# Performance work log

Hardware: AMD Instinct MI355X
Metric: run time of the kernel (lower is better)

## Reference

```python
import jax, jax.numpy as jnp
import numpy as np

N = 100_000   # nodes
E = 1_600_000 # edges
G = 128       # graphs in batch
DIN, DOUT = 100, 200


def setup_inputs() -> dict:
    key = jax.random.key(0)
    ks = jax.random.split(key, 12)
    def lin_w(k, fan_in, fan_out):
        return (jax.random.normal(k, (fan_in, fan_out), jnp.float32) / np.sqrt(fan_in)).astype(jnp.float32)
    return {
        "x": jax.random.normal(ks[0], (N, DIN), jnp.float32),
        "edge_index": jax.random.randint(ks[1], (2, E), 0, N, dtype=jnp.int32),
        "batch": jnp.sort(jax.random.randint(ks[2], (N,), 0, G, dtype=jnp.int32)),
        "W1": lin_w(ks[3], DIN, DOUT),  "b1": jnp.zeros((DOUT,), jnp.float32),
        "Wc": lin_w(ks[4], DOUT, DOUT), "bc": jnp.zeros((DOUT,), jnp.float32),
        "W2": lin_w(ks[5], DOUT, DOUT), "b2": jnp.zeros((DOUT,), jnp.float32),
        "W3": lin_w(ks[6], DOUT, DOUT), "b3": jnp.zeros((DOUT,), jnp.float32),
        "Wcls": lin_w(ks[7], DOUT, 2),  "bcls": jnp.zeros((2,), jnp.float32),
    }


def gcn_conv(x, W, b, src, dst, n_nodes):
    """PyG GCNConv: D^{-1/2}(A+I)D^{-1/2} X W + b, symmetric norm with self-loops."""
    h = x @ W  # [N, Dout]
    # degree at targets including the self-loop (+1)
    deg = jax.ops.segment_sum(jnp.ones((src.shape[0],), x.dtype), dst, num_segments=n_nodes) + 1.0
    dinv = jax.lax.rsqrt(deg)  # [N]
    # gather -> normalize -> scatter-add (messages along edges)
    msg = h[src] * (dinv[src] * dinv[dst])[:, None]          # [E, Dout]
    agg = jax.ops.segment_sum(msg, dst, num_segments=n_nodes)  # [N, Dout]
    # self-loop contribution handled analytically: norm_ii = dinv[i]^2
    agg = agg + h * (dinv * dinv)[:, None]
    return agg + b


def reference(x, edge_index, batch, W1, b1, Wc, bc, W2, b2, W3, b3, Wcls, bcls):
    src, dst = edge_index[0], edge_index[1]
    h = jax.nn.relu(gcn_conv(x, W1, b1, src, dst, N))
    # dropout is identity at eval time
    h = h @ Wc + bc
    h = jax.nn.relu(gcn_conv(h, W2, b2, src, dst, N))
    h = gcn_conv(h, W3, b3, src, dst, N)
    pooled = jax.ops.segment_max(h, batch, num_segments=G)  # global max pool -> [G, Dout]
    logits = pooled @ Wcls + bcls
    return jax.nn.softmax(logits, axis=1)
```

## Files before the change

### kernel.cpp

```cpp
#include <hip/hip_runtime.h>
#include <stdint.h>

#define N_NODES 100000
#define N_EDGES 1600000
#define N_GRAPHS 128
#define DIN 100
#define DOUT 200
#define LDH 200
#define LDX 128

#define NB 391
#define BCAP 5120
#define EPB 2048
#define NBLK 782

typedef unsigned short u16;
typedef unsigned int u32;
typedef _Float16 f16;
typedef f16 half8 __attribute__((ext_vector_type(8)));
typedef f16 half4 __attribute__((ext_vector_type(4)));
typedef f16 half2v __attribute__((ext_vector_type(2)));
typedef float floatx4 __attribute__((ext_vector_type(4)));

__device__ __forceinline__ float h2f(u16 h) {
  f16 x; __builtin_memcpy(&x, &h, 2); return (float)x;
}
__device__ __forceinline__ u16 f2h(float f) {
  f16 x = (f16)f; u16 r; __builtin_memcpy(&r, &x, 2); return r;
}

__device__ __forceinline__ void pack_frag(const float* __restrict__ W, int K, int nfrag,
                                          u16* __restrict__ out, int idx) {
  if (idx >= nfrag) return;
  int lane = idx & 63;
  int t = idx >> 6;
  int ct = t % 13, ks = t / 13;
  int n = ct * 16 + (lane & 15);
  int kbase = ks * 32 + (lane >> 4) * 8;
  u16 v[8];
  #pragma unroll
  for (int j = 0; j < 8; ++j) {
    int k = kbase + j;
    float f = (k < K && n < DOUT) ? W[(size_t)k * DOUT + n] : 0.f;
    v[j] = f2h(f);
  }
  uint4 o;
  o.x = (u32)v[0] | ((u32)v[1] << 16);
  o.y = (u32)v[2] | ((u32)v[3] << 16);
  o.z = (u32)v[4] | ((u32)v[5] << 16);
  o.w = (u32)v[6] | ((u32)v[7] << 16);
  *(uint4*)(out + (size_t)idx * 8) = o;
}

#define B_GB    391
#define B_COMB  549
#define B_PK1   562
#define B_PK3   585
#define B_TOT   (585 + NBLK)
__global__ void k_prep(const int* __restrict__ batch, int* __restrict__ gstart,
                       int* __restrict__ gend, const int* __restrict__ dst,
                       int* __restrict__ histAll,
                       const float* __restrict__ Wc, const float* __restrict__ bc,
                       const float* __restrict__ W2, float* __restrict__ Wc2,
                       float* __restrict__ bc2, const float* __restrict__ W1,
                       const float* __restrict__ W3, u16* __restrict__ Wpk1,
                       u16* __restrict__ Wpk3) {
  int b = blockIdx.x, t = threadIdx.x;
  if (b < B_GB) {
    int i = b * 256 + t;
    if (i >= N_NODES) return;
    int g = batch[i];
    if (i == 0 || batch[i - 1] != g) gstart[g] = i;
    if (i == N_NODES - 1 || batch[i + 1] != g) gend[g] = i;
  } else if (b < B_COMB) {
    int gid = (b - B_GB) * 256 + t;
    if (gid >= 201 * DOUT) return;
    int r = gid / DOUT, c = gid % DOUT;
    const float* a = (r < DOUT) ? (Wc + (size_t)r * DOUT) : bc;
    float s = 0.f;
    for (int k = 0; k < DOUT; ++k) s += a[k] * W2[(size_t)k * DOUT + c];
    if (r < DOUT) Wc2[(size_t)r * DOUT + c] = s;
    else bc2[c] = s;
  } else if (b < B_PK1) {
    pack_frag(W1, DIN, 4 * 13 * 64, Wpk1, (b - B_COMB) * 256 + t);
  } else if (b < B_PK3) {
    pack_frag(W3, DOUT, 7 * 13 * 64, Wpk3, (b - B_PK1) * 256 + t);
  } else {
    __shared__ int hist[NB];
    int hb = b - B_PK3;
    int e0 = hb * EPB;
    int e1 = min(e0 + EPB, N_EDGES);
    for (int j = t; j < NB; j += 256) hist[j] = 0;
    __syncthreads();
    for (int i = e0 + t; i < e1; i += 256)
      atomicAdd(&hist[dst[i] >> 8], 1);
    __syncthreads();
    for (int j = t; j < NB; j += 256)
      histAll[(size_t)hb * NB + j] = hist[j];
  }
}

__global__ void k_scan(const int* __restrict__ histAll, int* __restrict__ baseAll,
                       int* __restrict__ gcur) {
  __shared__ int s[256];
  int j = blockIdx.x, t = threadIdx.x;
  int run = 0;
  for (int c = 0; c < NBLK; c += 256) {
    int idx = c + t;
    int v = (idx < NBLK) ? histAll[(size_t)idx * NB + j] : 0;
    s[t] = v;
    __syncthreads();
    for (int o = 1; o < 256; o <<= 1) {
      int x = (t >= o) ? s[t - o] : 0;
      __syncthreads();
      s[t] += x;
      __syncthreads();
    }
    if (idx < NBLK) baseAll[(size_t)idx * NB + j] = run + s[t] - v;
    run += s[255];
    __syncthreads();
  }
  if (t == 0) gcur[j] = run;
}

__global__ void k_scatter(const int* __restrict__ src, const int* __restrict__ dst,
                          const int* __restrict__ baseAll, uint2* __restrict__ ebuf) {
  __shared__ int cur[NB];
  int b = blockIdx.x, t = threadIdx.x;
  int e0 = b * EPB;
  int e1 = min(e0 + EPB, N_EDGES);
  for (int j = t; j < NB; j += 256) cur[j] = baseAll[(size_t)b * NB + j];
  __syncthreads();
  for (int i = e0 + t; i < e1; i += 256) {
    int d = dst[i];
    int bk = d >> 8;
    int pos = atomicAdd(&cur[bk], 1);
    if (pos < BCAP)
      ebuf[(size_t)bk * BCAP + pos] = make_uint2((u32)d, (u32)src[i]);
  }
}

__global__ void k_csr(const uint2* __restrict__ ebuf, const int* __restrict__ gcur,
                      int* __restrict__ rowptr, float* __restrict__ dinv,
                      int* __restrict__ colv) {
  __shared__ int s_cnt[256];
  __shared__ int s_cur[256];
  __shared__ int s_scan[256];
  __shared__ int s_g[NB];
  __shared__ int s_base;
  int b = blockIdx.x, t = threadIdx.x;
  for (int j = t; j < NB; j += 256) s_g[j] = gcur[j];
  s_cnt[t] = 0;
  __syncthreads();
  if (t == 0) {
    int run = 0;
    for (int i = 0; i < b; ++i) run += s_g[i];
    s_base = run;
    if (b == NB - 1) rowptr[N_NODES] = run + s_g[b];
  }
  __syncthreads();
  int cnt = s_g[b];
  int base = s_base;
  int node0 = b << 8;
  const uint2* eb = ebuf + (size_t)b * BCAP;
  for (int i = t; i < cnt; i += 256)
    atomicAdd(&s_cnt[eb[i].x & 255], 1);
  __syncthreads();
  int v = s_cnt[t];
  s_scan[t] = v;
  __syncthreads();
  for (int o = 1; o < 256; o <<= 1) {
    int x = (t >= o) ? s_scan[t - o] : 0;
    __syncthreads();
    s_scan[t] += x;
    __syncthreads();
  }
  int run = s_scan[t] - v;
  s_cur[t] = base + run;
  int node = node0 + t;
  if (node < N_NODES) {
    rowptr[node] = base + run;
    dinv[node] = rsqrtf((float)v + 1.0f);
  }
  __syncthreads();
  for (int i = t; i < cnt; i += 256) {
    uint2 e = eb[i];
    int pos = atomicAdd(&s_cur[e.x & 255], 1);
    colv[pos] = (int)e.y;
  }
}

#define P_XS  25000
#define P_TOT 25023
__global__ void k_post(const float* __restrict__ x, const float* __restrict__ dinv,
                       u16* __restrict__ xs, const float* __restrict__ Wc2,
                       u16* __restrict__ Wpk2) {
  int b = blockIdx.x, t = threadIdx.x;
  if (b < P_XS) {
    int gid = b * 256 + t;
    int node = gid >> 6, lane = gid & 63;
    if (node >= N_NODES) return;
    if (lane >= 50) {
      int c = 100 + (lane - 50) * 2;
      *(half2v*)(xs + (size_t)node * LDX + c) = half2v{0, 0};
      return;
    }
    float d = dinv[node];
    float2 vv = *(const float2*)(x + (size_t)node * DIN + lane * 2);
    half2v o; o[0] = (f16)(d * vv.x); o[1] = (f16)(d * vv.y);
    *(half2v*)(xs + (size_t)node * LDX + lane * 2) = o;
  } else {
    pack_frag(Wc2, DOUT, 7 * 13 * 64, Wpk2, (b - P_XS) * 256 + t);
  }
}

template <int NKS>
__global__ __launch_bounds__(256) void k_gemm_mfma(const u16* __restrict__ A, int lda,
                                                   const u16* __restrict__ Wpk,
                                                   const float* __restrict__ bias,
                                                   const float* __restrict__ rowscale,
                                                   u16* __restrict__ C, int relu, int nrows) {
  int wv = threadIdx.x >> 6;
  int lane = threadIdx.x & 63;
  int r0 = blockIdx.x * 128 + wv * 32;
  int m = lane & 15, q = lane >> 4;
  int row0 = r0 + m, row1 = r0 + 16 + m;
  bool ok0 = (row0 < nrows), ok1 = (row1 < nrows);
  const u16* a0p = A + (size_t)row0 * lda + q * 8;
  const u16* a1p = A + (size_t)row1 * lda + q * 8;

  floatx4 acc0[13], acc1[13];
  #pragma unroll
  for (int ct = 0; ct < 13; ++ct) {
    acc0[ct] = floatx4{0.f, 0.f, 0.f, 0.f};
    acc1[ct] = floatx4{0.f, 0.f, 0.f, 0.f};
  }

  const u16* wp = Wpk + (size_t)lane * 8;
  #pragma unroll
  for (int ks = 0; ks < NKS; ++ks) {
    half8 a0 = ok0 ? *(const half8*)(a0p + ks * 32) : half8{0, 0, 0, 0, 0, 0, 0, 0};
    half8 a1 = ok1 ? *(const half8*)(a1p + ks * 32) : half8{0, 0, 0, 0, 0, 0, 0, 0};
    #pragma unroll
    for (int ct = 0; ct < 13; ++ct) {
      half8 bfr = *(const half8*)(wp + (size_t)(ks * 13 + ct) * 512);
      acc0[ct] = __builtin_amdgcn_mfma_f32_16x16x32_f16(a0, bfr, acc0[ct], 0, 0, 0);
      acc1[ct] = __builtin_amdgcn_mfma_f32_16x16x32_f16(a1, bfr, acc1[ct], 0, 0, 0);
    }
  }

  float sc0[4], sc1[4];
  #pragma unroll
  for (int rg = 0; rg < 4; ++rg) {
    int or0 = r0 + q * 4 + rg;
    int or1 = r0 + 16 + q * 4 + rg;
    sc0[rg] = (rowscale && or0 < nrows) ? rowscale[or0] : 1.f;
    sc1[rg] = (rowscale && or1 < nrows) ? rowscale[or1] : 1.f;
  }

  #pragma unroll
  for (int ct = 0; ct < 13; ++ct) {
    int c = ct * 16 + m;
    if (c >= DOUT) continue;
    float bv = bias ? bias[c] : 0.f;
    #pragma unroll
    for (int rg = 0; rg < 4; ++rg) {
      int or0 = r0 + q * 4 + rg;
      if (or0 < nrows) {
        float v = acc0[ct][rg] + bv;
        if (relu) v = fmaxf(v, 0.f);
        C[(size_t)or0 * LDH + c] = f2h(v * sc0[rg]);
      }
      int or1 = r0 + 16 + q * 4 + rg;
      if (or1 < nrows) {
        float v = acc1[ct][rg] + bv;
        if (relu) v = fmaxf(v, 0.f);
        C[(size_t)or1 * LDH + c] = f2h(v * sc1[rg]);
      }
    }
  }
}

__global__ void k_agg200h(const u16* __restrict__ T, const float* __restrict__ dinv,
                          const int* __restrict__ rowptr, const int* __restrict__ col,
                          const float* __restrict__ bias, u16* __restrict__ OUT,
                          int relu) {
  int wave = (blockIdx.x * blockDim.x + threadIdx.x) >> 6;
  int lane = threadIdx.x & 63;
  if (wave >= N_NODES || lane >= 50) return;
  int node = wave;
  int c4 = lane * 4;
  int beg = __builtin_amdgcn_readfirstlane(rowptr[node]);
  int end = __builtin_amdgcn_readfirstlane(rowptr[node + 1]);
  half4 sv = *(const half4*)(T + (size_t)node * LDH + c4);
  float di = dinv[node];
  float ax = 0.f, ay = 0.f, az = 0.f, aw = 0.f;
  int e = beg;
  for (; e + 16 <= end; e += 16) {
    int s[16];
    half4 tv[16];
    #pragma unroll
    for (int j = 0; j < 16; ++j) s[j] = col[e + j];
    #pragma unroll
    for (int j = 0; j < 16; ++j)
      tv[j] = *(const half4*)(T + (size_t)s[j] * LDH + c4);
    #pragma unroll
    for (int j = 0; j < 16; ++j) {
      ax += (float)tv[j][0]; ay += (float)tv[j][1];
      az += (float)tv[j][2]; aw += (float)tv[j][3];
    }
  }
  if (e + 8 <= end) {
    int s[8];
    half4 tv[8];
    #pragma unroll
    for (int j = 0; j < 8; ++j) s[j] = col[e + j];
    #pragma unroll
    for (int j = 0; j < 8; ++j)
      tv[j] = *(const half4*)(T + (size_t)s[j] * LDH + c4);
    #pragma unroll
    for (int j = 0; j < 8; ++j) {
      ax += (float)tv[j][0]; ay += (float)tv[j][1];
      az += (float)tv[j][2]; aw += (float)tv[j][3];
    }
    e += 8;
  }
  if (e + 4 <= end) {
    int s[4];
    half4 tv[4];
    #pragma unroll
    for (int j = 0; j < 4; ++j) s[j] = col[e + j];
    #pragma unroll
    for (int j = 0; j < 4; ++j)
      tv[j] = *(const half4*)(T + (size_t)s[j] * LDH + c4);
    #pragma unroll
    for (int j = 0; j < 4; ++j) {
      ax += (float)tv[j][0]; ay += (float)tv[j][1];
      az += (float)tv[j][2]; aw += (float)tv[j][3];
    }
    e += 4;
  }
  for (; e < end; ++e) {
    half4 tv = *(const half4*)(T + (size_t)col[e] * LDH + c4);
    ax += (float)tv[0]; ay += (float)tv[1];
    az += (float)tv[2]; aw += (float)tv[3];
  }
  float rx = di * (ax + (float)sv[0]);
  float ry = di * (ay + (float)sv[1]);
  float rz = di * (az + (float)sv[2]);
  float rw = di * (aw + (float)sv[3]);
  if (bias) {
    rx += bias[c4 + 0]; ry += bias[c4 + 1];
    rz += bias[c4 + 2]; rw += bias[c4 + 3];
  }
  if (relu) {
    rx = fmaxf(rx, 0.f); ry = fmaxf(ry, 0.f);
    rz = fmaxf(rz, 0.f); rw = fmaxf(rw, 0.f);
  }
  half4 o;
  o[0] = (f16)rx; o[1] = (f16)ry; o[2] = (f16)rz; o[3] = (f16)rw;
  __builtin_nontemporal_store(o, (half4*)(OUT + (size_t)node * LDH + c4));
}

__global__ void k_agg100h(const u16* __restrict__ T, const float* __restrict__ dinv,
                          const int* __restrict__ rowptr, const int* __restrict__ col,
                          u16* __restrict__ OUT) {
  int wave = (blockIdx.x * blockDim.x + threadIdx.x) >> 6;
  int lane = threadIdx.x & 63;
  if (wave >= N_NODES) return;
  int node = wave;
  int c2 = lane * 2;
  int beg = __builtin_amdgcn_readfirstlane(rowptr[node]);
  int end = __builtin_amdgcn_readfirstlane(rowptr[node + 1]);
  half2v sv = *(const half2v*)(T + (size_t)node * LDX + c2);
  float di = dinv[node];
  float ax = 0.f, ay = 0.f;
  int e = beg;
  for (; e + 16 <= end; e += 16) {
    int s[16];
    half2v tv[16];
    #pragma unroll
    for (int j = 0; j < 16; ++j) s[j] = col[e + j];
    #pragma unroll
    for (int j = 0; j < 16; ++j)
      tv[j] = *(const half2v*)(T + (size_t)s[j] * LDX + c2);
    #pragma unroll
    for (int j = 0; j < 16; ++j) { ax += (float)tv[j][0]; ay += (float)tv[j][1]; }
  }
  if (e + 8 <= end) {
    int s[8];
    half2v tv[8];
    #pragma unroll
    for (int j = 0; j < 8; ++j) s[j] = col[e + j];
    #pragma unroll
    for (int j = 0; j < 8; ++j)
      tv[j] = *(const half2v*)(T + (size_t)s[j] * LDX + c2);
    #pragma unroll
    for (int j = 0; j < 8; ++j) { ax += (float)tv[j][0]; ay += (float)tv[j][1]; }
    e += 8;
  }
  if (e + 4 <= end) {
    int s[4];
    half2v tv[4];
    #pragma unroll
    for (int j = 0; j < 4; ++j) s[j] = col[e + j];
    #pragma unroll
    for (int j = 0; j < 4; ++j)
      tv[j] = *(const half2v*)(T + (size_t)s[j] * LDX + c2);
    #pragma unroll
    for (int j = 0; j < 4; ++j) { ax += (float)tv[j][0]; ay += (float)tv[j][1]; }
    e += 4;
  }
  for (; e < end; ++e) {
    half2v tv = *(const half2v*)(T + (size_t)col[e] * LDX + c2);
    ax += (float)tv[0]; ay += (float)tv[1];
  }
  half2v o;
  o[0] = (f16)(di * (ax + (float)sv[0]));
  o[1] = (f16)(di * (ay + (float)sv[1]));
  __builtin_nontemporal_store(o, (half2v*)(OUT + (size_t)node * LDX + c2));
}

#define POOL_CHUNKS 8
__global__ void k_pool1h(const u16* __restrict__ H, const int* __restrict__ gstart,
                         const int* __restrict__ gend, float* __restrict__ part) {
  int g = blockIdx.x, c = blockIdx.y, t = threadIdx.x;
  if (t >= DOUT) return;
  int s = gstart[g], e = gend[g];
  float m = -3.4e38f;
  if (s >= 0 && e >= s && e < N_NODES) {
    int len = e - s + 1;
    int cs = s + (int)(((long long)len * c) / POOL_CHUNKS);
    int ce = s + (int)(((long long)len * (c + 1)) / POOL_CHUNKS);
    for (int i = cs; i < ce; ++i) m = fmaxf(m, h2f(H[(size_t)i * LDH + t]));
  }
  part[(size_t)(g * POOL_CHUNKS + c) * DOUT + t] = m;
}

__global__ void k_poolcls(const float* __restrict__ part, const float* __restrict__ Wcls,
                          const float* __restrict__ bcls, float* __restrict__ out) {
  __shared__ float l0s[256], l1s[256];
  int g = blockIdx.x, t = threadIdx.x;
  float c0 = 0.f, c1 = 0.f;
  if (t < DOUT) {
    float m = -3.4e38f;
    #pragma unroll
    for (int c = 0; c < POOL_CHUNKS; ++c)
      m = fmaxf(m, part[(size_t)(g * POOL_CHUNKS + c) * DOUT + t]);
    c0 = m * Wcls[t * 2 + 0];
    c1 = m * Wcls[t * 2 + 1];
  }
  l0s[t] = c0; l1s[t] = c1;
  __syncthreads();
  for (int o = 128; o > 0; o >>= 1) {
    if (t < o) { l0s[t] += l0s[t + o]; l1s[t] += l1s[t + o]; }
    __syncthreads();
  }
  if (t == 0) {
    float l0 = l0s[0] + bcls[0], l1 = l1s[0] + bcls[1];
    float m = fmaxf(l0, l1);
    float e0 = expf(l0 - m), e1 = expf(l1 - m);
    float inv = 1.0f / (e0 + e1);
    out[g * 2 + 0] = e0 * inv;
    out[g * 2 + 1] = e1 * inv;
  }
}

static inline size_t align256(size_t x) { return (x + 255) & ~(size_t)255; }

extern "C" void kernel_launch(void* const* d_in, const int* in_sizes, int n_in,
                              void* d_out, int out_size, void* d_ws, size_t ws_size,
                              hipStream_t stream) {
  const float* x     = (const float*)d_in[0];
  const int*   ei    = (const int*)d_in[1];
  const int*   batch = (const int*)d_in[2];
  const float* W1    = (const float*)d_in[3];
  const float* b1    = (const float*)d_in[4];
  const float* Wc    = (const float*)d_in[5];
  const float* bc    = (const float*)d_in[6];
  const float* W2    = (const float*)d_in[7];
  const float* b2    = (const float*)d_in[8];
  const float* W3    = (const float*)d_in[9];
  const float* b3    = (const float*)d_in[10];
  const float* Wcls  = (const float*)d_in[11];
  const float* bcls  = (const float*)d_in[12];
  float* out = (float*)d_out;

  const int N = N_NODES, E = N_EDGES;
  const int* src = ei;
  const int* dst = ei + E;

  char* ws = (char*)d_ws;
  size_t off = 0;
  float* dinv    = (float*)(ws + off); off = align256(off + (size_t)N * 4);
  int*   rowptr  = (int*)  (ws + off); off = align256(off + (size_t)(N + 1) * 4);
  int*   col     = (int*)  (ws + off); off = align256(off + (size_t)E * 4);
  int*   gcur    = (int*)  (ws + off); off = align256(off + (size_t)NB * 4);
  int*   histAll = (int*)  (ws + off); off = align256(off + (size_t)NBLK * NB * 4);
  int*   baseAll = (int*)  (ws + off); off = align256(off + (size_t)NBLK * NB * 4);
  int*   gstart  = (int*)  (ws + off); off = align256(off + 512);
  int*   gend    = (int*)  (ws + off); off = align256(off + 512);
  float* Wc2     = (float*)(ws + off); off = align256(off + (size_t)DOUT * DOUT * 4);
  float* bc2     = (float*)(ws + off); off = align256(off + (size_t)DOUT * 4);
  u16*   Wpk1    = (u16*)  (ws + off); off = align256(off + (size_t)4 * 13 * 64 * 8 * 2);
  u16*   Wpk2    = (u16*)  (ws + off); off = align256(off + (size_t)7 * 13 * 64 * 8 * 2);
  u16*   Wpk3    = (u16*)  (ws + off); off = align256(off + (size_t)7 * 13 * 64 * 8 * 2);
  u16*   xs      = (u16*)  (ws + off); off = align256(off + ((size_t)N * LDX + 128) * 2);
  u16*   bufX    = (u16*)  (ws + off); off = align256(off + ((size_t)N * LDX + 128) * 2);
  u16*   buf0    = (u16*)  (ws + off); off = align256(off + ((size_t)N * LDH + 128) * 2);
  u16*   buf1    = (u16*)  (ws + off); off = align256(off + ((size_t)N * LDH + 128) * 2);
  u16*   buf2    = (u16*)  (ws + off); off = align256(off + ((size_t)N * LDH + 128) * 2);

  uint2* ebuf = (uint2*)buf0;
  float* part = (float*)buf1;

  k_prep<<<B_TOT, 256, 0, stream>>>(batch, gstart, gend, dst, histAll,
                                    Wc, bc, W2, Wc2, bc2, W1, W3, Wpk1, Wpk3);
  k_scan<<<NB, 256, 0, stream>>>(histAll, baseAll, gcur);
  k_scatter<<<NBLK, 256, 0, stream>>>(src, dst, baseAll, ebuf);
  k_csr<<<NB, 256, 0, stream>>>(ebuf, gcur, rowptr, dinv, col);
  k_post<<<P_TOT, 256, 0, stream>>>(x, dinv, xs, Wc2, Wpk2);

  int gemmb = (N + 127) / 128;
  int aggb  = (N + 3) / 4;

  k_agg100h<<<aggb, 256, 0, stream>>>(xs, dinv, rowptr, col, bufX);
  k_gemm_mfma<4><<<gemmb, 256, 0, stream>>>(bufX, LDX, Wpk1, b1, nullptr, buf0, 1, N);
  k_gemm_mfma<7><<<gemmb, 256, 0, stream>>>(buf0, LDH, Wpk2, bc2, dinv, buf2, 0, N);
  k_agg200h<<<aggb, 256, 0, stream>>>(buf2, dinv, rowptr, col, b2, buf0, 1);
  k_gemm_mfma<7><<<gemmb, 256, 0, stream>>>(buf0, LDH, Wpk3, nullptr, dinv, buf1, 0, N);
  k_agg200h<<<aggb, 256, 0, stream>>>(buf1, dinv, rowptr, col, b3, buf2, 0);

  dim3 pg(N_GRAPHS, POOL_CHUNKS);
  k_pool1h<<<pg, 256, 0, stream>>>(buf2, gstart, gend, part);
  k_poolcls<<<N_GRAPHS, 256, 0, stream>>>(part, Wcls, bcls, out);
}
```

Before: 662.6 us.

## Process four nodes per wave in aggregation and parallelize CSR base sum

Each aggregation wave now handles four consecutive nodes. It loads their row pointers with one per-lane read and broadcasts them with readlane, which cuts wave count and per-node launch and setup overhead. The serial prefix sum for the CSR block base becomes a block-wide tree reduction. Pooling reads half2 pairs per thread. The zero-fill of padding columns in the scaled input is dropped, and aggregation lanes 50 and up now exit early, so padding columns in xs and bufX are never written. Those columns may then hold garbage that reaches the first GEMM, and NaN garbage multiplied by zero weights would still give NaN.

```diff
diff --git a/kernel.cpp b/kernel.cpp
--- a/kernel.cpp
+++ b/kernel.cpp
@@ -147,20 +147,22 @@
   __shared__ int s_cur[256];
   __shared__ int s_scan[256];
   __shared__ int s_g[NB];
-  __shared__ int s_base;
+  __shared__ int s_red[256];
   int b = blockIdx.x, t = threadIdx.x;
   for (int j = t; j < NB; j += 256) s_g[j] = gcur[j];
   s_cnt[t] = 0;
   __syncthreads();
-  if (t == 0) {
-    int run = 0;
-    for (int i = 0; i < b; ++i) run += s_g[i];
-    s_base = run;
-    if (b == NB - 1) rowptr[N_NODES] = run + s_g[b];
-  }
-  __syncthreads();
+  int pacc = 0;
+  for (int i = t; i < b; i += 256) pacc += s_g[i];
+  s_red[t] = pacc;
+  __syncthreads();
+  for (int o = 128; o > 0; o >>= 1) {
+    if (t < o) s_red[t] += s_red[t + o];
+    __syncthreads();
+  }
+  int base = s_red[0];
+  if (b == NB - 1 && t == 0) rowptr[N_NODES] = base + s_g[b];
   int cnt = s_g[b];
-  int base = s_base;
   int node0 = b << 8;
   const uint2* eb = ebuf + (size_t)b * BCAP;
   for (int i = t; i < cnt; i += 256)
@@ -199,12 +201,7 @@
   if (b < P_XS) {
     int gid = b * 256 + t;
     int node = gid >> 6, lane = gid & 63;
-    if (node >= N_NODES) return;
-    if (lane >= 50) {
-      int c = 100 + (lane - 50) * 2;
-      *(half2v*)(xs + (size_t)node * LDX + c) = half2v{0, 0};
-      return;
-    }
+    if (node >= N_NODES || lane >= 50) return;
     float d = dinv[node];
     float2 vv = *(const float2*)(x + (size_t)node * DIN + lane * 2);
     half2v o; o[0] = (f16)(d * vv.x); o[1] = (f16)(d * vv.y);
@@ -287,79 +284,84 @@
                           int relu) {
   int wave = (blockIdx.x * blockDim.x + threadIdx.x) >> 6;
   int lane = threadIdx.x & 63;
-  if (wave >= N_NODES || lane >= 50) return;
-  int node = wave;
+  int n0 = wave * 4;
+  if (n0 >= N_NODES) return;
+  int rpl = rowptr[n0 + (lane < 4 ? lane : 4)];
+  if (lane >= 50) return;
   int c4 = lane * 4;
-  int beg = __builtin_amdgcn_readfirstlane(rowptr[node]);
-  int end = __builtin_amdgcn_readfirstlane(rowptr[node + 1]);
-  half4 sv = *(const half4*)(T + (size_t)node * LDH + c4);
-  float di = dinv[node];
-  float ax = 0.f, ay = 0.f, az = 0.f, aw = 0.f;
-  int e = beg;
-  for (; e + 16 <= end; e += 16) {
-    int s[16];
-    half4 tv[16];
-    #pragma unroll
-    for (int j = 0; j < 16; ++j) s[j] = col[e + j];
-    #pragma unroll
-    for (int j = 0; j < 16; ++j)
-      tv[j] = *(const half4*)(T + (size_t)s[j] * LDH + c4);
-    #pragma unroll
-    for (int j = 0; j < 16; ++j) {
-      ax += (float)tv[j][0]; ay += (float)tv[j][1];
-      az += (float)tv[j][2]; aw += (float)tv[j][3];
-    }
-  }
-  if (e + 8 <= end) {
-    int s[8];
-    half4 tv[8];
-    #pragma unroll
-    for (int j = 0; j < 8; ++j) s[j] = col[e + j];
-    #pragma unroll
-    for (int j = 0; j < 8; ++j)
-      tv[j] = *(const half4*)(T + (size_t)s[j] * LDH + c4);
-    #pragma unroll
-    for (int j = 0; j < 8; ++j) {
-      ax += (float)tv[j][0]; ay += (float)tv[j][1];
-      az += (float)tv[j][2]; aw += (float)tv[j][3];
-    }
-    e += 8;
-  }
-  if (e + 4 <= end) {
-    int s[4];
-    half4 tv[4];
-    #pragma unroll
-    for (int j = 0; j < 4; ++j) s[j] = col[e + j];
-    #pragma unroll
-    for (int j = 0; j < 4; ++j)
-      tv[j] = *(const half4*)(T + (size_t)s[j] * LDH + c4);
-    #pragma unroll
-    for (int j = 0; j < 4; ++j) {
-      ax += (float)tv[j][0]; ay += (float)tv[j][1];
-      az += (float)tv[j][2]; aw += (float)tv[j][3];
-    }
-    e += 4;
-  }
-  for (; e < end; ++e) {
-    half4 tv = *(const half4*)(T + (size_t)col[e] * LDH + c4);
-    ax += (float)tv[0]; ay += (float)tv[1];
-    az += (float)tv[2]; aw += (float)tv[3];
-  }
-  float rx = di * (ax + (float)sv[0]);
-  float ry = di * (ay + (float)sv[1]);
-  float rz = di * (az + (float)sv[2]);
-  float rw = di * (aw + (float)sv[3]);
-  if (bias) {
-    rx += bias[c4 + 0]; ry += bias[c4 + 1];
-    rz += bias[c4 + 2]; rw += bias[c4 + 3];
-  }
-  if (relu) {
-    rx = fmaxf(rx, 0.f); ry = fmaxf(ry, 0.f);
-    rz = fmaxf(rz, 0.f); rw = fmaxf(rw, 0.f);
-  }
-  half4 o;
-  o[0] = (f16)rx; o[1] = (f16)ry; o[2] = (f16)rz; o[3] = (f16)rw;
-  __builtin_nontemporal_store(o, (half4*)(OUT + (size_t)node * LDH + c4));
+  for (int i = 0; i < 4; ++i) {
+    int node = n0 + i;
+    int beg = __builtin_amdgcn_readlane(rpl, i);
+    int end = __builtin_amdgcn_readlane(rpl, i + 1);
+    half4 sv = *(const half4*)(T + (size_t)node * LDH + c4);
+    float di = dinv[node];
+    float ax = 0.f, ay = 0.f, az = 0.f, aw = 0.f;
+    int e = beg;
+    for (; e + 16 <= end; e += 16) {
+      int s[16];
+      half4 tv[16];
+      #pragma unroll
+      for (int j = 0; j < 16; ++j) s[j] = col[e + j];
+      #pragma unroll
+      for (int j = 0; j < 16; ++j)
+        tv[j] = *(const half4*)(T + (size_t)s[j] * LDH + c4);
+      #pragma unroll
+      for (int j = 0; j < 16; ++j) {
+        ax += (float)tv[j][0]; ay += (float)tv[j][1];
+        az += (float)tv[j][2]; aw += (float)tv[j][3];
+      }
+    }
+    if (e + 8 <= end) {
+      int s[8];
+      half4 tv[8];
+      #pragma unroll
+      for (int j = 0; j < 8; ++j) s[j] = col[e + j];
+      #pragma unroll
+      for (int j = 0; j < 8; ++j)
+        tv[j] = *(const half4*)(T + (size_t)s[j] * LDH + c4);
+      #pragma unroll
+      for (int j = 0; j < 8; ++j) {
+        ax += (float)tv[j][0]; ay += (float)tv[j][1];
+        az += (float)tv[j][2]; aw += (float)tv[j][3];
+      }
+      e += 8;
+    }
+    if (e + 4 <= end) {
+      int s[4];
+      half4 tv[4];
+      #pragma unroll
+      for (int j = 0; j < 4; ++j) s[j] = col[e + j];
+      #pragma unroll
+      for (int j = 0; j < 4; ++j)
+        tv[j] = *(const half4*)(T + (size_t)s[j] * LDH + c4);
+      #pragma unroll
+      for (int j = 0; j < 4; ++j) {
+        ax += (float)tv[j][0]; ay += (float)tv[j][1];
+        az += (float)tv[j][2]; aw += (float)tv[j][3];
+      }
+      e += 4;
+    }
+    for (; e < end; ++e) {
+      half4 tv = *(const half4*)(T + (size_t)col[e] * LDH + c4);
+      ax += (float)tv[0]; ay += (float)tv[1];
+      az += (float)tv[2]; aw += (float)tv[3];
+    }
+    float rx = di * (ax + (float)sv[0]);
+    float ry = di * (ay + (float)sv[1]);
+    float rz = di * (az + (float)sv[2]);
+    float rw = di * (aw + (float)sv[3]);
+    if (bias) {
+      rx += bias[c4 + 0]; ry += bias[c4 + 1];
+      rz += bias[c4 + 2]; rw += bias[c4 + 3];
+    }
+    if (relu) {
+      rx = fmaxf(rx, 0.f); ry = fmaxf(ry, 0.f);
+      rz = fmaxf(rz, 0.f); rw = fmaxf(rw, 0.f);
+    }
+    half4 o;
+    o[0] = (f16)rx; o[1] = (f16)ry; o[2] = (f16)rz; o[3] = (f16)rw;
+    __builtin_nontemporal_store(o, (half4*)(OUT + (size_t)node * LDH + c4));
+  }
 }
 
 __global__ void k_agg100h(const u16* __restrict__ T, const float* __restrict__ dinv,
@@ -367,74 +369,85 @@
                           u16* __restrict__ OUT) {
   int wave = (blockIdx.x * blockDim.x + threadIdx.x) >> 6;
   int lane = threadIdx.x & 63;
-  if (wave >= N_NODES) return;
-  int node = wave;
+  int n0 = wave * 4;
+  if (n0 >= N_NODES) return;
+  int rpl = rowptr[n0 + (lane < 4 ? lane : 4)];
+  if (lane >= 50) return;
   int c2 = lane * 2;
-  int beg = __builtin_amdgcn_readfirstlane(rowptr[node]);
-  int end = __builtin_amdgcn_readfirstlane(rowptr[node + 1]);
-  half2v sv = *(const half2v*)(T + (size_t)node * LDX + c2);
-  float di = dinv[node];
-  float ax = 0.f, ay = 0.f;
-  int e = beg;
-  for (; e + 16 <= end; e += 16) {
-    int s[16];
-    half2v tv[16];
-    #pragma unroll
-    for (int j = 0; j < 16; ++j) s[j] = col[e + j];
-    #pragma unroll
-    for (int j = 0; j < 16; ++j)
-      tv[j] = *(const half2v*)(T + (size_t)s[j] * LDX + c2);
-    #pragma unroll
-    for (int j = 0; j < 16; ++j) { ax += (float)tv[j][0]; ay += (float)tv[j][1]; }
-  }
-  if (e + 8 <= end) {
-    int s[8];
-    half2v tv[8];
-    #pragma unroll
-    for (int j = 0; j < 8; ++j) s[j] = col[e + j];
-    #pragma unroll
-    for (int j = 0; j < 8; ++j)
-      tv[j] = *(const half2v*)(T + (size_t)s[j] * LDX + c2);
-    #pragma unroll
-    for (int j = 0; j < 8; ++j) { ax += (float)tv[j][0]; ay += (float)tv[j][1]; }
-    e += 8;
-  }
-  if (e + 4 <= end) {
-    int s[4];
-    half2v tv[4];
-    #pragma unroll
-    for (int j = 0; j < 4; ++j) s[j] = col[e + j];
-    #pragma unroll
-    for (int j = 0; j < 4; ++j)
-      tv[j] = *(const half2v*)(T + (size_t)s[j] * LDX + c2);
-    #pragma unroll
-    for (int j = 0; j < 4; ++j) { ax += (float)tv[j][0]; ay += (float)tv[j][1]; }
-    e += 4;
-  }
-  for (; e < end; ++e) {
-    half2v tv = *(const half2v*)(T + (size_t)col[e] * LDX + c2);
-    ax += (float)tv[0]; ay += (float)tv[1];
-  }
-  half2v o;
-  o[0] = (f16)(di * (ax + (float)sv[0]));
-  o[1] = (f16)(di * (ay + (float)sv[1]));
-  __builtin_nontemporal_store(o, (half2v*)(OUT + (size_t)node * LDX + c2));
+  for (int i = 0; i < 4; ++i) {
+    int node = n0 + i;
+    int beg = __builtin_amdgcn_readlane(rpl, i);
+    int end = __builtin_amdgcn_readlane(rpl, i + 1);
+    half2v sv = *(const half2v*)(T + (size_t)node * LDX + c2);
+    float di = dinv[node];
+    float ax = 0.f, ay = 0.f;
+    int e = beg;
+    for (; e + 16 <= end; e += 16) {
+      int s[16];
+      half2v tv[16];
+      #pragma unroll
+      for (int j = 0; j < 16; ++j) s[j] = col[e + j];
+      #pragma unroll
+      for (int j = 0; j < 16; ++j)
+        tv[j] = *(const half2v*)(T + (size_t)s[j] * LDX + c2);
+      #pragma unroll
+      for (int j = 0; j < 16; ++j) { ax += (float)tv[j][0]; ay += (float)tv[j][1]; }
+    }
+    if (e + 8 <= end) {
+      int s[8];
+      half2v tv[8];
+      #pragma unroll
+      for (int j = 0; j < 8; ++j) s[j] = col[e + j];
+      #pragma unroll
+      for (int j = 0; j < 8; ++j)
+        tv[j] = *(const half2v*)(T + (size_t)s[j] * LDX + c2);
+      #pragma unroll
+      for (int j = 0; j < 8; ++j) { ax += (float)tv[j][0]; ay += (float)tv[j][1]; }
+      e += 8;
+    }
+    if (e + 4 <= end) {
+      int s[4];
+      half2v tv[4];
+      #pragma unroll
+      for (int j = 0; j < 4; ++j) s[j] = col[e + j];
+      #pragma unroll
+      for (int j = 0; j < 4; ++j)
+        tv[j] = *(const half2v*)(T + (size_t)s[j] * LDX + c2);
+      #pragma unroll
+      for (int j = 0; j < 4; ++j) { ax += (float)tv[j][0]; ay += (float)tv[j][1]; }
+      e += 4;
+    }
+    for (; e < end; ++e) {
+      half2v tv = *(const half2v*)(T + (size_t)col[e] * LDX + c2);
+      ax += (float)tv[0]; ay += (float)tv[1];
+    }
+    half2v o;
+    o[0] = (f16)(di * (ax + (float)sv[0]));
+    o[1] = (f16)(di * (ay + (float)sv[1]));
+    __builtin_nontemporal_store(o, (half2v*)(OUT + (size_t)node * LDX + c2));
+  }
 }
 
 #define POOL_CHUNKS 8
 __global__ void k_pool1h(const u16* __restrict__ H, const int* __restrict__ gstart,
                          const int* __restrict__ gend, float* __restrict__ part) {
   int g = blockIdx.x, c = blockIdx.y, t = threadIdx.x;
-  if (t >= DOUT) return;
+  if (t >= 100) return;
   int s = gstart[g], e = gend[g];
-  float m = -3.4e38f;
+  float m0 = -3.4e38f, m1 = -3.4e38f;
   if (s >= 0 && e >= s && e < N_NODES) {
     int len = e - s + 1;
     int cs = s + (int)(((long long)len * c) / POOL_CHUNKS);
     int ce = s + (int)(((long long)len * (c + 1)) / POOL_CHUNKS);
-    for (int i = cs; i < ce; ++i) m = fmaxf(m, h2f(H[(size_t)i * LDH + t]));
-  }
-  part[(size_t)(g * POOL_CHUNKS + c) * DOUT + t] = m;
+    for (int i = cs; i < ce; ++i) {
+      half2v v = *(const half2v*)(H + (size_t)i * LDH + t * 2);
+      m0 = fmaxf(m0, (float)v[0]);
+      m1 = fmaxf(m1, (float)v[1]);
+    }
+  }
+  float* p = part + (size_t)(g * POOL_CHUNKS + c) * DOUT;
+  p[t * 2 + 0] = m0;
+  p[t * 2 + 1] = m1;
 }
 
 __global__ void k_poolcls(const float* __restrict__ part, const float* __restrict__ Wcls,
@@ -522,7 +535,7 @@
   k_post<<<P_TOT, 256, 0, stream>>>(x, dinv, xs, Wc2, Wpk2);
 
   int gemmb = (N + 127) / 128;
-  int aggb  = (N + 3) / 4;
+  int aggb  = (N + 15) / 16;
 
   k_agg100h<<<aggb, 256, 0, stream>>>(xs, dinv, rowptr, col, bufX);
   k_gemm_mfma<4><<<gemmb, 256, 0, stream>>>(bufX, LDX, Wpk1, b1, nullptr, buf0, 1, N);
```

Result: slower. 684.4 us (+3.3%).
